# Kernel tuning notes

Measured on AMD Instinct MI355X. Metric: run time of the kernel, lower is better.

Reference implementation:

```python
import jax, jax.numpy as jnp
import numpy as np

V = 36      # nodes per graph (3 temporal x 12 spatial)
C = 3       # temporal embedding slots
S = 12      # spatial embedding slots
F0 = 1025   # input feature width
H1, H2 = 256, 64
B = 1024    # graphs
N = B * V
DEG = 8     # random in-block neighbors per node (symmetrized -> 16 avg degree)
BN_EPS = 1e-5


def _edges(k):
    # 8 random neighbors per node within its own 36-node block, symmetrized
    nbr = jax.random.randint(k, (N, DEG), 0, V)
    block = (jnp.arange(N) // V) * V
    dst = (nbr + block[:, None]).reshape(-1)
    src = jnp.repeat(jnp.arange(N), DEG)
    return jnp.stack([jnp.concatenate([src, dst]),
                      jnp.concatenate([dst, src])]).astype(jnp.int32)


def setup_inputs() -> dict:
    k = jax.random.split(jax.random.key(0), 40)
    lin = lambda kk, i, o: (jax.random.normal(kk, (i, o), jnp.float32) / np.sqrt(i)).astype(jnp.float32)
    d = {}
    d['xF'] = jax.random.normal(k[0], (N, F0), jnp.float32)
    d['xD'] = jax.random.normal(k[1], (N, F0), jnp.float32)
    d['edge_index_F'] = _edges(k[2])
    d['edge_index_D'] = _edges(k[3])
    d['TembF'] = jax.random.normal(k[4], (C, F0), jnp.float32)
    d['SembF'] = jax.random.normal(k[5], (S, F0), jnp.float32)
    d['TembD'] = jax.random.normal(k[6], (C, F0), jnp.float32)
    d['SembD'] = jax.random.normal(k[7], (S, F0), jnp.float32)
    # ChebConv K=2 weights (Theta_0, Theta_1), biases; BatchNorm gamma/beta
    d['W0F1'] = lin(k[8], F0, H1); d['W1F1'] = lin(k[9], F0, H1); d['bF1'] = jnp.zeros((H1,), jnp.float32)
    d['gF1'] = jnp.ones((H1,), jnp.float32); d['btF1'] = jnp.zeros((H1,), jnp.float32)
    d['W0F2'] = lin(k[10], H1, H2); d['W1F2'] = lin(k[11], H1, H2); d['bF2'] = jnp.zeros((H2,), jnp.float32)
    d['gF2'] = jnp.ones((H2,), jnp.float32); d['btF2'] = jnp.zeros((H2,), jnp.float32)
    d['W0D1'] = lin(k[12], F0, H1); d['W1D1'] = lin(k[13], F0, H1); d['bD1'] = jnp.zeros((H1,), jnp.float32)
    d['gD1'] = jnp.ones((H1,), jnp.float32); d['btD1'] = jnp.zeros((H1,), jnp.float32)
    d['W0D2'] = lin(k[14], H1, H2); d['W1D2'] = lin(k[15], H1, H2); d['bD2'] = jnp.zeros((H2,), jnp.float32)
    d['gD2'] = jnp.ones((H2,), jnp.float32); d['btD2'] = jnp.zeros((H2,), jnp.float32)
    # fusion linear [256->5]; branch heads are tied-at-init clones of its halves
    Wlin = lin(k[16], 2 * (2 * H2), 5)
    blin = jnp.zeros((5,), jnp.float32)
    d['WlinF'] = Wlin[:2 * H2, :]; d['blinF'] = blin
    d['WlinD'] = Wlin[2 * H2:, :]; d['blinD'] = blin
    d['Wlin'] = Wlin; d['blin'] = blin
    return d


def _cheb(x, ei, W0, W1, b):
    # PyG ChebConv K=2, sym norm, lambda_max=2: out = x@W0 + (L_hat x)@W1 + b,
    # L_hat = -D^{-1/2} A D^{-1/2}. Transform-then-aggregate (linear, cheaper).
    n = x.shape[0]
    src, dst = ei[0], ei[1]
    deg = jax.ops.segment_sum(jnp.ones(src.shape, jnp.float32), src, n)
    dinv = jnp.where(deg > 0, jax.lax.rsqrt(jnp.maximum(deg, 1.0)), 0.0)
    w = -(dinv[src] * dinv[dst])                       # [E]
    h1 = x @ W1                                        # [N, out]
    tx1 = jax.ops.segment_sum(w[:, None] * h1[src], dst, n)  # scatter-add
    return x @ W0 + tx1 + b


def _bn_relu(x, g, bt):
    mu = x.mean(0)
    var = x.var(0)  # biased, as torch BatchNorm1d training-mode normalization
    return jax.nn.relu((x - mu) * jax.lax.rsqrt(var + BN_EPS) * g + bt)


def _branch(x, ei, Temb, Semb, W0a, W1a, ba, ga, bta, W0b, W1b, bb, gb, btb):
    n = x.shape[0]
    bsz = n // V
    x = x.reshape(bsz, C, S, F0).transpose(0, 2, 1, 3)      # [B,12,3,1025]
    x = x + Temb[None, None, :, :] + Semb[None, :, None, :]
    x = x.transpose(0, 2, 1, 3).reshape(n, F0)
    x = _bn_relu(_cheb(x, ei, W0a, W1a, ba), ga, bta)
    x = _bn_relu(_cheb(x, ei, W0b, W1b, bb), gb, btb)        # [N,64]
    # rows 12..23 of each 36-node block, pooled per graph
    idx = (jnp.arange(bsz)[:, None] * V + S + jnp.arange(S)[None, :]).reshape(-1)
    seg = jnp.repeat(jnp.arange(bsz), S)
    xs = x[idx]
    mx = jax.ops.segment_max(xs, seg, bsz)
    mn = jax.ops.segment_sum(xs, seg, bsz) / float(S)
    return jnp.concatenate([mx, mn], axis=1)                 # [B,128]


def reference(xF, xD, edge_index_F, edge_index_D, TembF, SembF, TembD, SembD,
              W0F1, W1F1, bF1, gF1, btF1, W0F2, W1F2, bF2, gF2, btF2,
              W0D1, W1D1, bD1, gD1, btD1, W0D2, W1D2, bD2, gD2, btD2,
              WlinF, blinF, WlinD, blinD, Wlin, blin):
    featF = _branch(xF, edge_index_F, TembF, SembF, W0F1, W1F1, bF1, gF1, btF1,
                    W0F2, W1F2, bF2, gF2, btF2)
    featD = _branch(xD, edge_index_D, TembD, SembD, W0D1, W1D1, bD1, gD1, btD1,
                    W0D2, W1D2, bD2, gD2, btD2)
    outF = jax.nn.softmax(featF @ WlinF + blinF, axis=-1)
    outD = jax.nn.softmax(featD @ WlinD + blinD, axis=-1)
    fusion = jnp.concatenate([featF, featD], axis=1)
    out = jax.nn.softmax(fusion @ Wlin + blin, axis=-1)
    return (outF, outD, fusion, out)
```

## Files before the change

kernel.cpp:

```cpp
#include <hip/hip_runtime.h>
#include <math.h>

#define NN    36864
#define F0    1025
#define H1D   256
#define H2D   64
#define VV    36
#define SS    12
#define BSZ   1024
#define BN_EPS 1e-5f

#define KT1   17
#define EMB_LD 1088
#define WT1_STRIDE  ((size_t)4*17*8192)
#define WT2_STRIDE  ((size_t)4*8192)

typedef __bf16 bf16x8 __attribute__((ext_vector_type(8)));
typedef __bf16 bf16x4 __attribute__((ext_vector_type(4)));
typedef float  f32x4  __attribute__((ext_vector_type(4)));

__device__ __forceinline__ float4 ld4u(const float* p) {
    float4 v;
    __builtin_memcpy(&v, p, 16);
    return v;
}

__global__ void k_zero(float* __restrict__ p, int n) {
    int i = blockIdx.x * blockDim.x + threadIdx.x;
    if (i < n) p[i] = 0.f;
}

__device__ __forceinline__ float dinv_f(float d) {
    return d > 0.f ? rsqrtf(fmaxf(d, 1.f)) : 0.f;
}

__global__ __launch_bounds__(128) void k_graph(
    const int* __restrict__ eiF, const int* __restrict__ eiD,
    int E, float* __restrict__ AdjAll) {
    __shared__ float deg_s[VV];
    __shared__ float Adj_s[VV * VV];
    int b = blockIdx.x, br = blockIdx.y, t = threadIdx.x;
    const int* e0 = br ? eiD : eiF;
    const int Eh = E / 2;
    const int base = b * VV;

    if (t < VV) deg_s[t] = 8.f;
    for (int i = t; i < VV * VV; i += 128) Adj_s[i] = 0.f;
    __syncthreads();

    for (int i = t; i < 288; i += 128) {
        int d = e0[Eh + b * 288 + i];
        atomicAdd(&deg_s[d - base], 1.f);
    }
    __syncthreads();

    for (int i = t; i < 576; i += 128) {
        int idx = (i < 288) ? (b * 288 + i) : (Eh + b * 288 + (i - 288));
        int s = e0[idx], d = e0[E + idx];
        float w = -dinv_f(deg_s[s - base]) * dinv_f(deg_s[d - base]);
        atomicAdd(&Adj_s[(d - base) * VV + (s - base)], w);
    }
    __syncthreads();

    float* A = AdjAll + ((size_t)br * BSZ + b) * (VV * VV);
    for (int i = t; i < VV * VV; i += 128) A[i] = Adj_s[i];
}

__global__ __launch_bounds__(256) void k_prepEmb(
    const float* __restrict__ TembF, const float* __restrict__ SembF,
    const float* __restrict__ TembD, const float* __restrict__ SembD,
    float* __restrict__ embSAll) {
    int br = blockIdx.y;
    const float* Temb = br ? TembD : TembF;
    const float* Semb = br ? SembD : SembF;
    float* out = embSAll + (size_t)br * VV * EMB_LD;
    int id = blockIdx.x * 256 + threadIdx.x;
    if (id >= VV * (EMB_LD / 4)) return;
    int lv = id / (EMB_LD / 4);
    int k0 = (id - lv * (EMB_LD / 4)) * 4;
    const float* pt = Temb + (size_t)(lv / SS) * F0;
    const float* ps = Semb + (size_t)(lv % SS) * F0;
    float4 v;
    float* vp = (float*)&v;
#pragma unroll
    for (int j = 0; j < 4; ++j) {
        int k = k0 + j;
        vp[j] = (k < F0) ? (pt[k] + ps[k]) : 0.f;
    }
    *reinterpret_cast<float4*>(out + (size_t)lv * EMB_LD + k0) = v;
}

__global__ __launch_bounds__(256) void k_prepW(
    const float* __restrict__ WaF, const float* __restrict__ WbF,
    const float* __restrict__ WaD, const float* __restrict__ WbD,
    __bf16* __restrict__ Wt, int K, int nkt, int split, int ldw, size_t brStride) {
    int br = blockIdx.y;
    const float* Wa = br ? WaD : WaF;
    const float* Wb = br ? WbD : WbF;
    __bf16* out = Wt + (size_t)br * brStride;

    int id = blockIdx.x * 256 + threadIdx.x;
    int gpc = nkt * 8;
    int c = id / gpc, gi = id - c * gpc;
    int kt = gi >> 3, g = gi & 7;
    int k0 = kt * 64 + g * 8;
    const float* src = (c < split) ? (Wa + c) : (Wb + (c - split));
    bf16x8 ov;
#pragma unroll
    for (int j = 0; j < 8; ++j) {
        int k = k0 + j;
        float v = (k < K) ? src[(size_t)k * ldw] : 0.f;
        ov[j] = (__bf16)v;
    }
    int r = c & 127, bn = c >> 7;
    size_t dst = ((size_t)(bn * nkt + kt) << 13) + r * 64 + ((g ^ (r & 7)) << 3);
    *(bf16x8*)(out + dst) = ov;
}

__global__ __launch_bounds__(512) void k_gemm1f(
    const float* __restrict__ xF, const float* __restrict__ xD,
    const float* __restrict__ embSAll,
    const __bf16* __restrict__ Wt1All,
    __bf16* __restrict__ H0All, __bf16* __restrict__ H1All) {
    __shared__ __align__(16) __bf16 As[2 * 8192];
    __shared__ __align__(16) __bf16 Bs[2 * 16384];
    const int tid = threadIdx.x;
    const int lane = tid & 63, wid = tid >> 6;

    const int flat = blockIdx.x;
    const int w = (flat & 7) * 144 + (flat >> 3);
    const int cy = w & 1;
    const int t2 = w >> 1;
    const int bm = t2 % 288;
    const int br = t2 / 288;

    const float* x    = br ? xD : xF;
    const float* embS = embSAll + (size_t)br * VV * EMB_LD;
    const __bf16* Wt = Wt1All + (size_t)br * WT1_STRIDE;
    __bf16* H0 = H0All + (size_t)br * NN * H1D;
    __bf16* H1 = H1All + (size_t)br * NN * H1D;

    const int wr = wid >> 2, wc = wid & 3;
    const int l15 = lane & 15, lg = lane >> 4;
    const int bn0 = cy * 2;

    const int kc = (lane & 15) * 4;
    const float *px[4], *pe[4];
    int dso[4];
#pragma unroll
    for (int i = 0; i < 4; ++i) {
        int r = wid * 16 + i * 4 + (lane >> 4);
        int g = bm * 128 + r;
        int lv = g % VV;
        px[i] = x + (size_t)g * F0 + kc;
        pe[i] = embS + (size_t)lv * EMB_LD + kc;
        dso[i] = r * 64 + (((kc >> 3) ^ (r & 7)) << 3) + (kc & 4);
    }

    int offA[2][4], offB[2][4];
#pragma unroll
    for (int kk = 0; kk < 2; ++kk) {
#pragma unroll
        for (int m = 0; m < 4; ++m) {
            int rowA = wr * 64 + m * 16 + l15;
            offA[kk][m] = rowA * 64 + (((kk * 4 + lg) ^ (rowA & 7)) << 3);
        }
#pragma unroll
        for (int n = 0; n < 4; ++n) {
            int col = wc * 64 + n * 16 + l15;
            offB[kk][n] = (col >> 7) * 8192 + (col & 127) * 64
                          + (((kk * 4 + lg) ^ (col & 7)) << 3);
        }
    }

    f32x4 acc[4][4];
#pragma unroll
    for (int m = 0; m < 4; ++m)
#pragma unroll
        for (int n = 0; n < 4; ++n) acc[m][n] = (f32x4){0.f, 0.f, 0.f, 0.f};

    f32x4 xa0[4], xa1[4];

    auto issueX = [&](int kt, f32x4 (&xa)[4]) {
        int ko = kt * 64, kb = ko + kc;
#pragma unroll
        for (int i = 0; i < 4; ++i) {
            if (kb + 3 < F0) {
                float4 a = ld4u(px[i] + ko);
                xa[i] = (f32x4){a.x, a.y, a.z, a.w};
            } else {
                f32x4 v = {0.f, 0.f, 0.f, 0.f};
#pragma unroll
                for (int j = 0; j < 4; ++j)
                    if (kb + j < F0) v[j] = px[i][ko + j];
                xa[i] = v;
            }
        }
    };
    auto writeA = [&](int kt, int buf, f32x4 (&xa)[4]) {
        int ko = kt * 64;
#pragma unroll
        for (int i = 0; i < 4; ++i) {
            float4 e = *reinterpret_cast<const float4*>(pe[i] + ko);
            bf16x4 wv;
            wv[0] = (__bf16)(xa[i][0] + e.x);
            wv[1] = (__bf16)(xa[i][1] + e.y);
            wv[2] = (__bf16)(xa[i][2] + e.z);
            wv[3] = (__bf16)(xa[i][3] + e.w);
            *(bf16x4*)(As + buf * 8192 + dso[i]) = wv;
        }
    };
    auto issueB = [&](int kt, int buf) {
#pragma unroll
        for (int cc = 0; cc < 4; ++cc) {
            int q = (wid * 4 + cc) * 512;
            int h = q >> 13, qi = q & 8191;
            const __bf16* src = Wt + (((size_t)(bn0 + h) * KT1 + kt) << 13)
                                + qi + (lane << 3);
            __builtin_amdgcn_global_load_lds(
                (const __attribute__((address_space(1))) void*)src,
                (__attribute__((address_space(3))) void*)(Bs + buf * 16384 + q), 16, 0, 0);
        }
    };
    auto mfmaStep = [&](int cur) {
        const __bf16* Ab = As + cur * 8192;
        const __bf16* Bb = Bs + cur * 16384;
#pragma unroll
        for (int kk = 0; kk < 2; ++kk) {
            bf16x8 af[4], bb[4];
#pragma unroll
            for (int m = 0; m < 4; ++m) af[m] = *(const bf16x8*)(Ab + offA[kk][m]);
#pragma unroll
            for (int n = 0; n < 4; ++n) bb[n] = *(const bf16x8*)(Bb + offB[kk][n]);
#pragma unroll
            for (int m = 0; m < 4; ++m)
#pragma unroll
                for (int n = 0; n < 4; ++n)
                    acc[m][n] = __builtin_amdgcn_mfma_f32_16x16x32_bf16(
                        af[m], bb[n], acc[m][n], 0, 0, 0);
        }
    };

    issueX(0, xa0);
    issueB(0, 0);
    writeA(0, 0, xa0);
    issueX(1, xa1);

    for (int kt = 0; kt < KT1; kt += 2) {
        __syncthreads();
        if (kt + 1 < KT1) issueB(kt + 1, 1);
        if (kt + 2 < KT1) issueX(kt + 2, xa0);
        mfmaStep(0);
        if (kt + 1 < KT1) writeA(kt + 1, 1, xa1);
        if (kt + 1 >= KT1) break;
        __syncthreads();
        if (kt + 2 < KT1) issueB(kt + 2, 0);
        if (kt + 3 < KT1) issueX(kt + 3, xa1);
        mfmaStep(1);
        if (kt + 2 < KT1) writeA(kt + 2, 0, xa0);
    }

    const int cr = lg * 4;
#pragma unroll
    for (int m = 0; m < 4; ++m) {
        int grow = bm * 128 + wr * 64 + m * 16 + cr;
#pragma unroll
        for (int n = 0; n < 4; ++n) {
            int gc = cy * 256 + wc * 64 + n * 16 + l15;
#pragma unroll
            for (int j = 0; j < 4; ++j) {
                int r = grow + j;
                if (gc < 256) H0[(size_t)r * H1D + gc] = (__bf16)acc[m][n][j];
                else          H1[(size_t)r * H1D + (gc - 256)] = (__bf16)acc[m][n][j];
            }
        }
    }
}

__global__ __launch_bounds__(256, 2) void k_gemm2f(
    const __bf16* __restrict__ YAll, const float* __restrict__ coefAll,
    const __bf16* __restrict__ Wt2All,
    float* __restrict__ G0All, __bf16* __restrict__ G1All) {
    __shared__ __align__(16) __bf16 As[2 * 8192];
    __shared__ __align__(16) __bf16 Bs[2 * 8192];
    const int tid = threadIdx.x;
    const int lane = tid & 63, wid = tid >> 6;
    const int bm = blockIdx.x, br = blockIdx.z;
    const __bf16* Y   = YAll + (size_t)br * NN * H1D;
    const float* coef = coefAll + (size_t)br * 2 * H1D;
    const __bf16* Wt  = Wt2All + (size_t)br * WT2_STRIDE;
    float*  G0 = G0All + (size_t)br * NN * H2D;
    __bf16* G1 = G1All + (size_t)br * NN * H2D;

    const int wr = wid >> 1, wc = wid & 1;
    const int l15 = lane & 15, lg = lane >> 4;

    const int kc = (lane & 15) * 4;
    const __bf16* pyr[8];
    int dso[8];
#pragma unroll
    for (int i = 0; i < 8; ++i) {
        int r = wid * 32 + i * 4 + (lane >> 4);
        pyr[i] = Y + (size_t)(bm * 128 + r) * H1D + kc;
        dso[i] = r * 64 + (((kc >> 3) ^ (r & 7)) << 3) + (kc & 4);
    }

    int offA[2][4], offB[2][4];
#pragma unroll
    for (int kk = 0; kk < 2; ++kk)
#pragma unroll
        for (int m = 0; m < 4; ++m) {
            int rowA = wr * 64 + m * 16 + l15;
            offA[kk][m] = rowA * 64 + (((kk * 4 + lg) ^ (rowA & 7)) << 3);
            int col = wc * 64 + m * 16 + l15;
            offB[kk][m] = col * 64 + (((kk * 4 + lg) ^ (col & 7)) << 3);
        }

    f32x4 acc[4][4];
#pragma unroll
    for (int m = 0; m < 4; ++m)
#pragma unroll
        for (int n = 0; n < 4; ++n) acc[m][n] = (f32x4){0.f, 0.f, 0.f, 0.f};

    bf16x4 ya[8];

    auto issueY = [&](int kt) {
        int k0 = kt * 64;
#pragma unroll
        for (int i = 0; i < 8; ++i)
            ya[i] = *reinterpret_cast<const bf16x4*>(pyr[i] + k0);
    };
    auto writeA = [&](int kt, int buf) {
        int k0 = kt * 64;
        float4 cA = *reinterpret_cast<const float4*>(coef + k0 + kc);
        float4 cB = *reinterpret_cast<const float4*>(coef + H1D + k0 + kc);
#pragma unroll
        for (int i = 0; i < 8; ++i) {
            bf16x4 wv;
            wv[0] = (__bf16)fmaxf(fmaf((float)ya[i][0], cA.x, cB.x), 0.f);
            wv[1] = (__bf16)fmaxf(fmaf((float)ya[i][1], cA.y, cB.y), 0.f);
            wv[2] = (__bf16)fmaxf(fmaf((float)ya[i][2], cA.z, cB.z), 0.f);
            wv[3] = (__bf16)fmaxf(fmaf((float)ya[i][3], cA.w, cB.w), 0.f);
            *(bf16x4*)(As + buf * 8192 + dso[i]) = wv;
        }
    };
    auto issueB = [&](int kt, int buf) {
#pragma unroll
        for (int cc = 0; cc < 4; ++cc) {
            int q = (wid * 4 + cc) * 512;
            const __bf16* src = Wt + ((size_t)kt << 13) + q + (lane << 3);
            __builtin_amdgcn_global_load_lds(
                (const __attribute__((address_space(1))) void*)src,
                (__attribute__((address_space(3))) void*)(Bs + buf * 8192 + q), 16, 0, 0);
        }
    };

    issueB(0, 0);
    issueY(0);
    writeA(0, 0);

    for (int kt = 0; kt < 4; ++kt) {
        const int cur = kt & 1, nxt = cur ^ 1;
        __syncthreads();
        if (kt + 1 < 4) {
            issueB(kt + 1, nxt);
            issueY(kt + 1);
        }
        const __bf16* Ab = As + cur * 8192;
        const __bf16* Bb = Bs + cur * 8192;
#pragma unroll
        for (int kk = 0; kk < 2; ++kk) {
            bf16x8 af[4], bb[4];
#pragma unroll
            for (int m = 0; m < 4; ++m) af[m] = *(const bf16x8*)(Ab + offA[kk][m]);
#pragma unroll
            for (int n = 0; n < 4; ++n) bb[n] = *(const bf16x8*)(Bb + offB[kk][n]);
#pragma unroll
            for (int m = 0; m < 4; ++m)
#pragma unroll
                for (int n = 0; n < 4; ++n)
                    acc[m][n] = __builtin_amdgcn_mfma_f32_16x16x32_bf16(
                        af[m], bb[n], acc[m][n], 0, 0, 0);
        }
        if (kt + 1 < 4) writeA(kt + 1, nxt);
    }

    const int cr = lg * 4;
#pragma unroll
    for (int m = 0; m < 4; ++m) {
        int grow = bm * 128 + wr * 64 + m * 16 + cr;
#pragma unroll
        for (int n = 0; n < 4; ++n) {
            int col = wc * 64 + n * 16 + l15;
#pragma unroll
            for (int j = 0; j < 4; ++j) {
                int r = grow + j;
                if (col < 64) G0[(size_t)r * H2D + col] = acc[m][n][j];
                else          G1[(size_t)r * H2D + (col - 64)] = (__bf16)acc[m][n][j];
            }
        }
    }
}

__global__ __launch_bounds__(256) void k_combine_stats1(
    const float* __restrict__ AdjAll, const __bf16* __restrict__ H1All,
    const float* __restrict__ bF, const float* __restrict__ bD,
    __bf16* __restrict__ YAll, float* __restrict__ stAll) {
    __shared__ float Adj_s[VV * VV];
    __shared__ float red[256 * 9];
    int b = blockIdx.x, br = blockIdx.y, t = threadIdx.x;
    const float* Adj = AdjAll + ((size_t)br * BSZ + b) * (VV * VV);
    const __bf16* h1 = H1All + ((size_t)br * NN + (size_t)b * VV) * H1D;
    __bf16* yb = YAll + ((size_t)br * NN + (size_t)b * VV) * H1D;
    float* st = stAll + (size_t)br * 2 * H1D;
    const float* bias = br ? bD : bF;

    for (int e = t; e < VV * VV; e += 256) Adj_s[e] = Adj[e];
    __syncthreads();

    int c0 = (t & 63) * 4, r0 = t >> 6;
    float4 bv = *reinterpret_cast<const float4*>(bias + c0);
    float acc[9][4];
#pragma unroll
    for (int i = 0; i < 9; ++i) {
        bf16x4 y = *reinterpret_cast<const bf16x4*>(yb + (size_t)(r0 + 4 * i) * H1D + c0);
        acc[i][0] = (float)y[0] + bv.x; acc[i][1] = (float)y[1] + bv.y;
        acc[i][2] = (float)y[2] + bv.z; acc[i][3] = (float)y[3] + bv.w;
    }
#pragma unroll 4
    for (int j = 0; j < VV; ++j) {
        bf16x4 hv = *reinterpret_cast<const bf16x4*>(h1 + (size_t)j * H1D + c0);
        float h0 = (float)hv[0], h1f = (float)hv[1], h2 = (float)hv[2], h3 = (float)hv[3];
#pragma unroll
        for (int i = 0; i < 9; ++i) {
            float a = Adj_s[(r0 + 4 * i) * VV + j];
            acc[i][0] = fmaf(a, h0, acc[i][0]);
            acc[i][1] = fmaf(a, h1f, acc[i][1]);
            acc[i][2] = fmaf(a, h2, acc[i][2]);
            acc[i][3] = fmaf(a, h3, acc[i][3]);
        }
    }
    float s[4] = {0, 0, 0, 0}, s2[4] = {0, 0, 0, 0};
#pragma unroll
    for (int i = 0; i < 9; ++i) {
        bf16x4 wv;
        wv[0] = (__bf16)acc[i][0]; wv[1] = (__bf16)acc[i][1];
        wv[2] = (__bf16)acc[i][2]; wv[3] = (__bf16)acc[i][3];
        *reinterpret_cast<bf16x4*>(yb + (size_t)(r0 + 4 * i) * H1D + c0) = wv;
#pragma unroll
        for (int k = 0; k < 4; ++k) { s[k] += acc[i][k]; s2[k] += acc[i][k] * acc[i][k]; }
    }
#pragma unroll
    for (int k = 0; k < 4; ++k) { red[t * 9 + k] = s[k]; red[t * 9 + 4 + k] = s2[k]; }
    __syncthreads();
    {
        int cg = t >> 2, k = t & 3;
        float ss = 0.f, ss2 = 0.f;
#pragma unroll
        for (int q = 0; q < 4; ++q) {
            ss  += red[(q * 64 + cg) * 9 + k];
            ss2 += red[(q * 64 + cg) * 9 + 4 + k];
        }
        atomicAdd(&st[t], ss);
        atomicAdd(&st[H1D + t], ss2);
    }
}

__global__ __launch_bounds__(256) void k_combine_stats2(
    const float* __restrict__ AdjAll, const __bf16* __restrict__ G1All,
    const float* __restrict__ bF, const float* __restrict__ bD,
    float* __restrict__ YAll, float* __restrict__ stAll) {
    __shared__ float Adj_s[VV * VV];
    __shared__ float red[256 * 9];
    int b = blockIdx.x, br = blockIdx.y, t = threadIdx.x;
    const float* Adj = AdjAll + ((size_t)br * BSZ + b) * (VV * VV);
    const __bf16* g1 = G1All + ((size_t)br * NN + (size_t)b * VV) * H2D;
    float* yb = YAll + ((size_t)br * NN + (size_t)b * VV) * H2D;
    float* st = stAll + (size_t)br * 2 * H2D;
    const float* bias = br ? bD : bF;

    for (int e = t; e < VV * VV; e += 256) Adj_s[e] = Adj[e];
    __syncthreads();

    int c0 = (t & 15) * 4, r0 = t >> 4;
    int nr = (r0 < 4) ? 3 : 2;
    float4 bv = *reinterpret_cast<const float4*>(bias + c0);
    float acc[3][4];
    for (int i = 0; i < nr; ++i) {
        float4 y = *reinterpret_cast<const float4*>(yb + (size_t)(r0 + 16 * i) * H2D + c0);
        acc[i][0] = y.x + bv.x; acc[i][1] = y.y + bv.y;
        acc[i][2] = y.z + bv.z; acc[i][3] = y.w + bv.w;
    }
#pragma unroll 4
    for (int j = 0; j < VV; ++j) {
        bf16x4 hv = *reinterpret_cast<const bf16x4*>(g1 + (size_t)j * H2D + c0);
        float h0 = (float)hv[0], h1f = (float)hv[1], h2 = (float)hv[2], h3 = (float)hv[3];
        for (int i = 0; i < nr; ++i) {
            float a = Adj_s[(r0 + 16 * i) * VV + j];
            acc[i][0] = fmaf(a, h0, acc[i][0]);
            acc[i][1] = fmaf(a, h1f, acc[i][1]);
            acc[i][2] = fmaf(a, h2, acc[i][2]);
            acc[i][3] = fmaf(a, h3, acc[i][3]);
        }
    }
    float s[4] = {0, 0, 0, 0}, s2[4] = {0, 0, 0, 0};
    for (int i = 0; i < nr; ++i) {
        *reinterpret_cast<float4*>(yb + (size_t)(r0 + 16 * i) * H2D + c0) =
            make_float4(acc[i][0], acc[i][1], acc[i][2], acc[i][3]);
#pragma unroll
        for (int k = 0; k < 4; ++k) { s[k] += acc[i][k]; s2[k] += acc[i][k] * acc[i][k]; }
    }
#pragma unroll
    for (int k = 0; k < 4; ++k) { red[t * 9 + k] = s[k]; red[t * 9 + 4 + k] = s2[k]; }
    __syncthreads();
    if (t < 2 * H2D) {
        int cg = (t & 63) >> 2, k = t & 3, which = t >> 6;
        float ss = 0.f;
#pragma unroll
        for (int q = 0; q < 16; ++q) ss += red[(q * 16 + cg) * 9 + which * 4 + k];
        atomicAdd(&st[(t >> 6) * H2D + (t & 63)], ss);
    }
}

__global__ void k_fin(const float* __restrict__ stAll,
                      const float* __restrict__ gF, const float* __restrict__ btF,
                      const float* __restrict__ gD, const float* __restrict__ btD,
                      float* __restrict__ coefAll, int H) {
    int br = blockIdx.x, t = threadIdx.x;
    const float* st = stAll + (size_t)br * 2 * H;
    float* coef = coefAll + (size_t)br * 2 * H;
    const float* g = br ? gD : gF;
    const float* bt = br ? btD : btF;
    if (t >= H) return;
    float mu = st[t] / (float)NN;
    float var = st[H + t] / (float)NN - mu * mu;
    float sA = g[t] * rsqrtf(var + BN_EPS);
    coef[t] = sA;
    coef[H + t] = bt[t] - mu * sA;
}

__global__ __launch_bounds__(128) void k_poolheads(
    const float* __restrict__ G0All, const float* __restrict__ coef2All,
    const float* __restrict__ WlinF, const float* __restrict__ blinF,
    const float* __restrict__ WlinD, const float* __restrict__ blinD,
    const float* __restrict__ Wlin, const float* __restrict__ blin,
    float* __restrict__ out) {
    __shared__ float sF[128], sD[128], lg[24];
    int r = blockIdx.x, t = threadIdx.x;

    {
        int br = t >> 6, c = t & 63;
        const float* Y2 = G0All + (size_t)br * NN * H2D;
        const float* coef = coef2All + (size_t)br * 2 * H2D;
        float sA = coef[c], sB = coef[H2D + c];
        float mx = -1e30f, sm = 0.f;
        const float* yb = Y2 + ((size_t)r * VV + SS) * H2D + c;
#pragma unroll
        for (int i = 0; i < SS; ++i) {
            float v = fmaxf(fmaf(yb[i * H2D], sA, sB), 0.f);
            mx = fmaxf(mx, v);
            sm += v;
        }
        float* feat = br ? sD : sF;
        feat[c] = mx;
        feat[64 + c] = sm * (1.f / 12.f);
    }
    __syncthreads();

    float* fus = out + 10240 + (size_t)r * 256;
    fus[t] = sF[t];
    fus[128 + t] = sD[t];
    if (t < 5) {
        float a = blinF[t];
        for (int k = 0; k < 128; ++k) a += sF[k] * WlinF[k * 5 + t];
        lg[t] = a;
    } else if (t >= 8 && t < 13) {
        int j = t - 8;
        float a = blinD[j];
        for (int k = 0; k < 128; ++k) a += sD[k] * WlinD[k * 5 + j];
        lg[8 + j] = a;
    } else if (t >= 16 && t < 21) {
        int j = t - 16;
        float a = blin[j];
        for (int k = 0; k < 128; ++k) a += sF[k] * Wlin[k * 5 + j];
        for (int k = 0; k < 128; ++k) a += sD[k] * Wlin[(128 + k) * 5 + j];
        lg[16 + j] = a;
    }
    __syncthreads();
    if (t < 15) {
        int grp = t / 5, j = t % 5;
        const float* l = &lg[grp * 8];
        float m = l[0];
#pragma unroll
        for (int k = 1; k < 5; ++k) m = fmaxf(m, l[k]);
        float den = 0.f;
#pragma unroll
        for (int k = 0; k < 5; ++k) den += expf(l[k] - m);
        float v = expf(l[j] - m) / den;
        float* dst = (grp == 0) ? out : (grp == 1 ? out + 5120 : out + 272384);
        dst[r * 5 + j] = v;
    }
}

extern "C" void kernel_launch(void* const* d_in, const int* in_sizes, int n_in,
                              void* d_out, int out_size, void* d_ws, size_t ws_size,
                              hipStream_t stream) {
    const float* xF    = (const float*)d_in[0];
    const float* xD    = (const float*)d_in[1];
    const int*   eiF   = (const int*)d_in[2];
    const int*   eiD   = (const int*)d_in[3];
    const float* TembF = (const float*)d_in[4];
    const float* SembF = (const float*)d_in[5];
    const float* TembD = (const float*)d_in[6];
    const float* SembD = (const float*)d_in[7];
    const float* W0F1  = (const float*)d_in[8];
    const float* W1F1  = (const float*)d_in[9];
    const float* bF1   = (const float*)d_in[10];
    const float* gF1   = (const float*)d_in[11];
    const float* btF1  = (const float*)d_in[12];
    const float* W0F2  = (const float*)d_in[13];
    const float* W1F2  = (const float*)d_in[14];
    const float* bF2   = (const float*)d_in[15];
    const float* gF2   = (const float*)d_in[16];
    const float* btF2  = (const float*)d_in[17];
    const float* W0D1  = (const float*)d_in[18];
    const float* W1D1  = (const float*)d_in[19];
    const float* bD1   = (const float*)d_in[20];
    const float* gD1   = (const float*)d_in[21];
    const float* btD1  = (const float*)d_in[22];
    const float* W0D2  = (const float*)d_in[23];
    const float* W1D2  = (const float*)d_in[24];
    const float* bD2   = (const float*)d_in[25];
    const float* gD2   = (const float*)d_in[26];
    const float* btD2  = (const float*)d_in[27];
    const float* WlinF = (const float*)d_in[28];
    const float* blinF = (const float*)d_in[29];
    const float* WlinD = (const float*)d_in[30];
    const float* blinD = (const float*)d_in[31];
    const float* Wlin  = (const float*)d_in[32];
    const float* blin  = (const float*)d_in[33];

    const int E = in_sizes[2] / 2;

    float* ws = (float*)d_ws;
    size_t o = 0;
    __bf16* H0bf = (__bf16*)(ws + o);   o += (size_t)2 * NN * H1D / 2;
    __bf16* H1bf = (__bf16*)(ws + o);   o += (size_t)2 * NN * H1D / 2;
    float*  G0   = ws + o;              o += (size_t)2 * NN * H2D;
    __bf16* G1bf = (__bf16*)(ws + o);   o += (size_t)2 * NN * H2D / 2;
    __bf16* Wt1  = (__bf16*)(ws + o);   o += (size_t)2 * WT1_STRIDE / 2;
    __bf16* Wt2  = (__bf16*)(ws + o);   o += (size_t)2 * WT2_STRIDE / 2;
    float*  embS = ws + o;              o += (size_t)2 * VV * EMB_LD;
    float*  Adj  = ws + o;              o += (size_t)2 * BSZ * VV * VV;
    float*  st1  = ws + o;              o += 2 * 2 * H1D;
    float*  st2  = ws + o;              o += 2 * 2 * H2D;
    float*  coef1 = ws + o;             o += 2 * 2 * H1D;
    float*  coef2 = ws + o;             o += 2 * 2 * H2D;

    const int zeroN = 2 * (2 * H1D + 2 * H2D);

    k_zero<<<(zeroN + 255) / 256, 256, 0, stream>>>(st1, zeroN);
    k_graph<<<dim3(BSZ, 2), 128, 0, stream>>>(eiF, eiD, E, Adj);
    k_prepEmb<<<dim3(39, 2), 256, 0, stream>>>(TembF, SembF, TembD, SembD, embS);
    k_prepW<<<dim3(272, 2), 256, 0, stream>>>(W0F1, W1F1, W0D1, W1D1, Wt1,
                                              F0, 17, 256, H1D, WT1_STRIDE);
    k_prepW<<<dim3(16, 2), 256, 0, stream>>>(W0F2, W1F2, W0D2, W1D2, Wt2,
                                             H1D, 4, 64, H2D, WT2_STRIDE);
    k_gemm1f<<<dim3(1152), 512, 0, stream>>>(xF, xD, embS, Wt1, H0bf, H1bf);
    k_combine_stats1<<<dim3(BSZ, 2), 256, 0, stream>>>(Adj, H1bf, bF1, bD1, H0bf, st1);
    k_fin<<<dim3(2), 256, 0, stream>>>(st1, gF1, btF1, gD1, btD1, coef1, H1D);
    k_gemm2f<<<dim3(288, 1, 2), 256, 0, stream>>>(H0bf, coef1, Wt2, G0, G1bf);
    k_combine_stats2<<<dim3(BSZ, 2), 256, 0, stream>>>(Adj, G1bf, bF2, bD2, G0, st2);
    k_fin<<<dim3(2), 64, 0, stream>>>(st2, gF2, btF2, gD2, btD2, coef2, H2D);
    k_poolheads<<<dim3(BSZ), 128, 0, stream>>>(G0, coef2, WlinF, blinF, WlinD, blinD,
                                               Wlin, blin, (float*)d_out);
}
```

Before: 409.0 us.

## Enlarge gemm1 M-tile to 192 rows and fold small kernels into neighbours

The first GEMM now uses 192-row tiles instead of 128 rows, so each block does 6x4 MFMA tiles per wave and fewer blocks re-read the weight tiles. The separate zeroing kernel is folded into k_graph, and the two BN-finalize kernels are removed: their coefficient computation is done inside k_gemm2f (into shared memory) and inside k_poolheads. This removes three launches and some weight reloads, at the cost of more registers and LDS per gemm1 block, which may reduce occupancy. With 768 blocks the grid is also less even across CUs.

```diff
diff --git a/kernel.cpp b/kernel.cpp
--- a/kernel.cpp
+++ b/kernel.cpp
@@ -25,24 +25,22 @@
     return v;
 }
 
-__global__ void k_zero(float* __restrict__ p, int n) {
-    int i = blockIdx.x * blockDim.x + threadIdx.x;
-    if (i < n) p[i] = 0.f;
-}
-
 __device__ __forceinline__ float dinv_f(float d) {
     return d > 0.f ? rsqrtf(fmaxf(d, 1.f)) : 0.f;
 }
 
 __global__ __launch_bounds__(128) void k_graph(
     const int* __restrict__ eiF, const int* __restrict__ eiD,
-    int E, float* __restrict__ AdjAll) {
+    int E, float* __restrict__ AdjAll, float* __restrict__ stAll) {
     __shared__ float deg_s[VV];
     __shared__ float Adj_s[VV * VV];
     int b = blockIdx.x, br = blockIdx.y, t = threadIdx.x;
     const int* e0 = br ? eiD : eiF;
     const int Eh = E / 2;
     const int base = b * VV;
+
+    if (b == 0 && br == 0)
+        for (int i = t; i < 2 * (2 * H1D + 2 * H2D) / 2 * 2; i += 128) stAll[i] = 0.f;
 
     if (t < VV) deg_s[t] = 8.f;
     for (int i = t; i < VV * VV; i += 128) Adj_s[i] = 0.f;
@@ -122,17 +120,17 @@
     const float* __restrict__ embSAll,
     const __bf16* __restrict__ Wt1All,
     __bf16* __restrict__ H0All, __bf16* __restrict__ H1All) {
-    __shared__ __align__(16) __bf16 As[2 * 8192];
+    __shared__ __align__(16) __bf16 As[2 * 12288];
     __shared__ __align__(16) __bf16 Bs[2 * 16384];
     const int tid = threadIdx.x;
     const int lane = tid & 63, wid = tid >> 6;
 
     const int flat = blockIdx.x;
-    const int w = (flat & 7) * 144 + (flat >> 3);
+    const int w = (flat & 7) * 96 + (flat >> 3);
     const int cy = w & 1;
     const int t2 = w >> 1;
-    const int bm = t2 % 288;
-    const int br = t2 / 288;
+    const int bm = t2 % 192;
+    const int br = t2 / 192;
 
     const float* x    = br ? xD : xF;
     const float* embS = embSAll + (size_t)br * VV * EMB_LD;
@@ -145,24 +143,24 @@
     const int bn0 = cy * 2;
 
     const int kc = (lane & 15) * 4;
-    const float *px[4], *pe[4];
-    int dso[4];
-#pragma unroll
-    for (int i = 0; i < 4; ++i) {
-        int r = wid * 16 + i * 4 + (lane >> 4);
-        int g = bm * 128 + r;
+    const float *px[6], *pe[6];
+    int dso[6];
+#pragma unroll
+    for (int i = 0; i < 6; ++i) {
+        int r = wid * 24 + i * 4 + (lane >> 4);
+        int g = bm * 192 + r;
         int lv = g % VV;
         px[i] = x + (size_t)g * F0 + kc;
         pe[i] = embS + (size_t)lv * EMB_LD + kc;
         dso[i] = r * 64 + (((kc >> 3) ^ (r & 7)) << 3) + (kc & 4);
     }
 
-    int offA[2][4], offB[2][4];
+    int offA[2][6], offB[2][4];
 #pragma unroll
     for (int kk = 0; kk < 2; ++kk) {
 #pragma unroll
-        for (int m = 0; m < 4; ++m) {
-            int rowA = wr * 64 + m * 16 + l15;
+        for (int m = 0; m < 6; ++m) {
+            int rowA = wr * 96 + m * 16 + l15;
             offA[kk][m] = rowA * 64 + (((kk * 4 + lg) ^ (rowA & 7)) << 3);
         }
 #pragma unroll
@@ -173,18 +171,18 @@
         }
     }
 
-    f32x4 acc[4][4];
-#pragma unroll
-    for (int m = 0; m < 4; ++m)
+    f32x4 acc[6][4];
+#pragma unroll
+    for (int m = 0; m < 6; ++m)
 #pragma unroll
         for (int n = 0; n < 4; ++n) acc[m][n] = (f32x4){0.f, 0.f, 0.f, 0.f};
 
-    f32x4 xa0[4], xa1[4];
-
-    auto issueX = [&](int kt, f32x4 (&xa)[4]) {
+    f32x4 xa0[6], xa1[6];
+
+    auto issueX = [&](int kt, f32x4 (&xa)[6]) {
         int ko = kt * 64, kb = ko + kc;
 #pragma unroll
-        for (int i = 0; i < 4; ++i) {
+        for (int i = 0; i < 6; ++i) {
             if (kb + 3 < F0) {
                 float4 a = ld4u(px[i] + ko);
                 xa[i] = (f32x4){a.x, a.y, a.z, a.w};
@@ -197,17 +195,17 @@
             }
         }
     };
-    auto writeA = [&](int kt, int buf, f32x4 (&xa)[4]) {
+    auto writeA = [&](int kt, int buf, f32x4 (&xa)[6]) {
         int ko = kt * 64;
 #pragma unroll
-        for (int i = 0; i < 4; ++i) {
+        for (int i = 0; i < 6; ++i) {
             float4 e = *reinterpret_cast<const float4*>(pe[i] + ko);
             bf16x4 wv;
             wv[0] = (__bf16)(xa[i][0] + e.x);
             wv[1] = (__bf16)(xa[i][1] + e.y);
             wv[2] = (__bf16)(xa[i][2] + e.z);
             wv[3] = (__bf16)(xa[i][3] + e.w);
-            *(bf16x4*)(As + buf * 8192 + dso[i]) = wv;
+            *(bf16x4*)(As + buf * 12288 + dso[i]) = wv;
         }
     };
     auto issueB = [&](int kt, int buf) {
@@ -223,17 +221,17 @@
         }
     };
     auto mfmaStep = [&](int cur) {
-        const __bf16* Ab = As + cur * 8192;
+        const __bf16* Ab = As + cur * 12288;
         const __bf16* Bb = Bs + cur * 16384;
 #pragma unroll
         for (int kk = 0; kk < 2; ++kk) {
-            bf16x8 af[4], bb[4];
-#pragma unroll
-            for (int m = 0; m < 4; ++m) af[m] = *(const bf16x8*)(Ab + offA[kk][m]);
+            bf16x8 af[6], bb[4];
+#pragma unroll
+            for (int m = 0; m < 6; ++m) af[m] = *(const bf16x8*)(Ab + offA[kk][m]);
 #pragma unroll
             for (int n = 0; n < 4; ++n) bb[n] = *(const bf16x8*)(Bb + offB[kk][n]);
 #pragma unroll
-            for (int m = 0; m < 4; ++m)
+            for (int m = 0; m < 6; ++m)
 #pragma unroll
                 for (int n = 0; n < 4; ++n)
                     acc[m][n] = __builtin_amdgcn_mfma_f32_16x16x32_bf16(
@@ -262,8 +260,8 @@
 
     const int cr = lg * 4;
 #pragma unroll
-    for (int m = 0; m < 4; ++m) {
-        int grow = bm * 128 + wr * 64 + m * 16 + cr;
+    for (int m = 0; m < 6; ++m) {
+        int grow = bm * 192 + wr * 96 + m * 16 + cr;
 #pragma unroll
         for (int n = 0; n < 4; ++n) {
             int gc = cy * 256 + wc * 64 + n * 16 + l15;
@@ -278,19 +276,34 @@
 }
 
 __global__ __launch_bounds__(256, 2) void k_gemm2f(
-    const __bf16* __restrict__ YAll, const float* __restrict__ coefAll,
+    const __bf16* __restrict__ YAll, const float* __restrict__ stAll,
+    const float* __restrict__ gF, const float* __restrict__ btF,
+    const float* __restrict__ gD, const float* __restrict__ btD,
     const __bf16* __restrict__ Wt2All,
     float* __restrict__ G0All, __bf16* __restrict__ G1All) {
     __shared__ __align__(16) __bf16 As[2 * 8192];
     __shared__ __align__(16) __bf16 Bs[2 * 8192];
+    __shared__ float coef_s[2 * H1D];
     const int tid = threadIdx.x;
     const int lane = tid & 63, wid = tid >> 6;
     const int bm = blockIdx.x, br = blockIdx.z;
     const __bf16* Y   = YAll + (size_t)br * NN * H1D;
-    const float* coef = coefAll + (size_t)br * 2 * H1D;
     const __bf16* Wt  = Wt2All + (size_t)br * WT2_STRIDE;
     float*  G0 = G0All + (size_t)br * NN * H2D;
     __bf16* G1 = G1All + (size_t)br * NN * H2D;
+
+    {
+        const float* st = stAll + (size_t)br * 2 * H1D;
+        const float* g  = br ? gD : gF;
+        const float* bt = br ? btD : btF;
+        int c = tid;
+        float mu = st[c] / (float)NN;
+        float var = st[H1D + c] / (float)NN - mu * mu;
+        float sA = g[c] * rsqrtf(var + BN_EPS);
+        coef_s[c] = sA;
+        coef_s[H1D + c] = bt[c] - mu * sA;
+    }
+    __syncthreads();
 
     const int wr = wid >> 1, wc = wid & 1;
     const int l15 = lane & 15, lg = lane >> 4;
@@ -332,8 +345,8 @@
     };
     auto writeA = [&](int kt, int buf) {
         int k0 = kt * 64;
-        float4 cA = *reinterpret_cast<const float4*>(coef + k0 + kc);
-        float4 cB = *reinterpret_cast<const float4*>(coef + H1D + k0 + kc);
+        float4 cA = *reinterpret_cast<const float4*>(coef_s + k0 + kc);
+        float4 cB = *reinterpret_cast<const float4*>(coef_s + H1D + k0 + kc);
 #pragma unroll
         for (int i = 0; i < 8; ++i) {
             bf16x4 wv;
@@ -522,25 +535,10 @@
     }
 }
 
-__global__ void k_fin(const float* __restrict__ stAll,
-                      const float* __restrict__ gF, const float* __restrict__ btF,
-                      const float* __restrict__ gD, const float* __restrict__ btD,
-                      float* __restrict__ coefAll, int H) {
-    int br = blockIdx.x, t = threadIdx.x;
-    const float* st = stAll + (size_t)br * 2 * H;
-    float* coef = coefAll + (size_t)br * 2 * H;
-    const float* g = br ? gD : gF;
-    const float* bt = br ? btD : btF;
-    if (t >= H) return;
-    float mu = st[t] / (float)NN;
-    float var = st[H + t] / (float)NN - mu * mu;
-    float sA = g[t] * rsqrtf(var + BN_EPS);
-    coef[t] = sA;
-    coef[H + t] = bt[t] - mu * sA;
-}
-
 __global__ __launch_bounds__(128) void k_poolheads(
-    const float* __restrict__ G0All, const float* __restrict__ coef2All,
+    const float* __restrict__ G0All, const float* __restrict__ st2All,
+    const float* __restrict__ gF2, const float* __restrict__ btF2,
+    const float* __restrict__ gD2, const float* __restrict__ btD2,
     const float* __restrict__ WlinF, const float* __restrict__ blinF,
     const float* __restrict__ WlinD, const float* __restrict__ blinD,
     const float* __restrict__ Wlin, const float* __restrict__ blin,
@@ -551,8 +549,13 @@
     {
         int br = t >> 6, c = t & 63;
         const float* Y2 = G0All + (size_t)br * NN * H2D;
-        const float* coef = coef2All + (size_t)br * 2 * H2D;
-        float sA = coef[c], sB = coef[H2D + c];
+        const float* st = st2All + (size_t)br * 2 * H2D;
+        const float* g  = br ? gD2 : gF2;
+        const float* bt = br ? btD2 : btF2;
+        float mu = st[c] / (float)NN;
+        float var = st[H2D + c] / (float)NN - mu * mu;
+        float sA = g[c] * rsqrtf(var + BN_EPS);
+        float sB = bt[c] - mu * sA;
         float mx = -1e30f, sm = 0.f;
         const float* yb = Y2 + ((size_t)r * VV + SS) * H2D + c;
 #pragma unroll
@@ -654,24 +657,19 @@
     float*  Adj  = ws + o;              o += (size_t)2 * BSZ * VV * VV;
     float*  st1  = ws + o;              o += 2 * 2 * H1D;
     float*  st2  = ws + o;              o += 2 * 2 * H2D;
-    float*  coef1 = ws + o;             o += 2 * 2 * H1D;
-    float*  coef2 = ws + o;             o += 2 * 2 * H2D;
-
-    const int zeroN = 2 * (2 * H1D + 2 * H2D);
-
-    k_zero<<<(zeroN + 255) / 256, 256, 0, stream>>>(st1, zeroN);
-    k_graph<<<dim3(BSZ, 2), 128, 0, stream>>>(eiF, eiD, E, Adj);
+
+    k_graph<<<dim3(BSZ, 2), 128, 0, stream>>>(eiF, eiD, E, Adj, st1);
     k_prepEmb<<<dim3(39, 2), 256, 0, stream>>>(TembF, SembF, TembD, SembD, embS);
     k_prepW<<<dim3(272, 2), 256, 0, stream>>>(W0F1, W1F1, W0D1, W1D1, Wt1,
                                               F0, 17, 256, H1D, WT1_STRIDE);
     k_prepW<<<dim3(16, 2), 256, 0, stream>>>(W0F2, W1F2, W0D2, W1D2, Wt2,
                                              H1D, 4, 64, H2D, WT2_STRIDE);
-    k_gemm1f<<<dim3(1152), 512, 0, stream>>>(xF, xD, embS, Wt1, H0bf, H1bf);
+    k_gemm1f<<<dim3(768), 512, 0, stream>>>(xF, xD, embS, Wt1, H0bf, H1bf);
     k_combine_stats1<<<dim3(BSZ, 2), 256, 0, stream>>>(Adj, H1bf, bF1, bD1, H0bf, st1);
-    k_fin<<<dim3(2), 256, 0, stream>>>(st1, gF1, btF1, gD1, btD1, coef1, H1D);
-    k_gemm2f<<<dim3(288, 1, 2), 256, 0, stream>>>(H0bf, coef1, Wt2, G0, G1bf);
+    k_gemm2f<<<dim3(288, 1, 2), 256, 0, stream>>>(H0bf, st1, gF1, btF1, gD1, btD1,
+                                                  Wt2, G0, G1bf);
     k_combine_stats2<<<dim3(BSZ, 2), 256, 0, stream>>>(Adj, G1bf, bF2, bD2, G0, st2);
-    k_fin<<<dim3(2), 64, 0, stream>>>(st2, gF2, btF2, gD2, btD2, coef2, H2D);
-    k_poolheads<<<dim3(BSZ), 128, 0, stream>>>(G0, coef2, WlinF, blinF, WlinD, blinD,
+    k_poolheads<<<dim3(BSZ), 128, 0, stream>>>(G0, st2, gF2, btF2, gD2, btD2,
+                                               WlinF, blinF, WlinD, blinD,
                                                Wlin, blin, (float*)d_out);
 }
```

New measurement: 776.5 us. +89.8%, slower.
